# Kernel tuning notes

Measured on AMD Instinct MI355X. Metric: run time of the kernel, lower is better.

The kernel has to match this reference:

```python
import jax, jax.numpy as jnp
import numpy as np

B, N = 8192, 128          # batch, num intruders
D_OWN, D_GRID, D_INTR = 16, 512, 20
H, OUT = 128, 4


def setup_inputs() -> dict:
    key = jax.random.key(0)
    ks = jax.random.split(key, 12)
    rn = lambda k, shape, s=1.0: jax.random.normal(k, shape, jnp.float32) * s
    return {
        "state0": rn(ks[0], (B, D_OWN)),
        "state1": rn(ks[1], (B, D_GRID)),
        "state2": rn(ks[2], (B, N, D_INTR)),
        "W_own": rn(ks[3], (D_OWN, H), 0.1), "b_own": jnp.zeros((H,), jnp.float32),
        "W_intr": rn(ks[4], (D_INTR, H), 0.1), "b_intr": jnp.zeros((H,), jnp.float32),
        "W_grid": rn(ks[5], (D_GRID, H), 0.05), "b_grid": jnp.zeros((H,), jnp.float32),
        "Wq": rn(ks[6], (H, H), 0.08),
        "Wk": rn(ks[7], (H, H), 0.08),
        "Wv": rn(ks[8], (H, H), 0.08),
        "W1": rn(ks[9], (3 * H, H), 0.05), "b1": jnp.zeros((H,), jnp.float32),
        "W2": rn(ks[10], (H, OUT), 0.1), "b2": jnp.zeros((OUT,), jnp.float32),
    }


def reference(state0, state1, state2, W_own, b_own, W_intr, b_intr,
              W_grid, b_grid, Wq, Wk, Wv, W1, b1, W2, b2):
    own_e = jax.nn.relu(state0 @ W_own + b_own)            # [B,H]
    x_e = jax.nn.relu(state2 @ W_intr + b_intr)            # [B,N,H]
    q = own_e @ Wq                                         # [B,H]
    k = x_e @ Wk                                           # [B,N,H]
    v = x_e @ Wv                                           # [B,N,H]
    # mask = state2.mean(axis=2, keepdim=True).bool()  (nonzero test)
    mask = jnp.mean(state2, axis=2, keepdims=True) != 0    # [B,N,1]
    score = jnp.einsum('bnh,bh->bn', k, q)[..., None]      # bmm(k, q.unsqueeze(2)) -> [B,N,1]
    score = jnp.where(mask, score, -jnp.inf)
    alpha = jax.nn.softmax(score / np.float32(np.sqrt(H)), axis=1)
    alpha = jnp.where(mask, alpha, 0.0)
    v_att = jnp.sum(v * alpha, axis=1)                     # [B,H]
    own_grid = jax.nn.relu(state1 @ W_grid + b_grid)       # [B,H]
    concat = jnp.concatenate([own_e, v_att, own_grid], axis=1)  # [B,3H]
    out = (concat @ W1 + b1) @ W2 + b2                     # action_out_SAC
    mean = out
    log_std = jnp.clip(out, -20.0, 2.0)
    return mean, log_std
```

## Files before the change

kernel.cpp:

```cpp
#include <hip/hip_runtime.h>

typedef unsigned short ushort_t;
typedef __attribute__((ext_vector_type(8))) short bf16x8;
typedef __attribute__((ext_vector_type(4))) float f32x4;

__device__ __forceinline__ float bflo(unsigned u) { return __uint_as_float(u << 16); }
__device__ __forceinline__ float bfhi(unsigned u) { return __uint_as_float(u & 0xffff0000u); }
__device__ __forceinline__ float bfu(ushort_t s)  { return __uint_as_float((unsigned)s << 16); }
__device__ __forceinline__ ushort_t f2bf(float f) {
    unsigned u = __float_as_uint(f);
    u = u + 0x7fffu + ((u >> 16) & 1u);
    return (ushort_t)(u >> 16);
}
__device__ __forceinline__ void unpack8(uint4 v, float* f) {
    f[0]=bflo(v.x); f[1]=bfhi(v.x); f[2]=bflo(v.y); f[3]=bfhi(v.y);
    f[4]=bflo(v.z); f[5]=bfhi(v.z); f[6]=bflo(v.w); f[7]=bfhi(v.w);
}

__device__ __forceinline__ float load1(const void* p, size_t i, int f32) {
    return f32 ? ((const float*)p)[i] : bfu(((const ushort_t*)p)[i]);
}
__device__ __forceinline__ void load8(const void* p, size_t i, int f32, float* f) {
    if (f32) {
        const float4 a = *(const float4*)((const float*)p + i);
        const float4 b = *(const float4*)((const float*)p + i + 4);
        f[0]=a.x; f[1]=a.y; f[2]=a.z; f[3]=a.w;
        f[4]=b.x; f[5]=b.y; f[6]=b.z; f[7]=b.w;
    } else {
        unpack8(*(const uint4*)((const ushort_t*)p + i), f);
    }
}
__device__ __forceinline__ void load4(const void* p, size_t i, int f32, float* f) {
    if (f32) {
        const float4 a = *(const float4*)((const float*)p + i);
        f[0]=a.x; f[1]=a.y; f[2]=a.z; f[3]=a.w;
    } else {
        const uint2 u = *(const uint2*)((const ushort_t*)p + i);
        f[0]=bflo(u.x); f[1]=bfhi(u.x); f[2]=bflo(u.y); f[3]=bfhi(u.y);
    }
}

__device__ __forceinline__ int detect_f32(const ushort_t* s1h) {
    const int ln = threadIdx.x & 63;
    float v = fmaxf(fabsf(bfu(s1h[ln])), fabsf(bfu(s1h[ln + 64])));
    bool big = !(v <= 1e6f);
    return __ballot(big) != 0ull;
}

#define B_TOT 8192

__device__ __attribute__((aligned(16))) float    g_M[128 * 128];
__device__ __attribute__((aligned(16))) float    g_Wc1[384 * 4];
__device__ __attribute__((aligned(16))) float    g_Wv2[128 * 4];
__device__ __attribute__((aligned(16))) float    g_bc[4];
__device__ __attribute__((aligned(16))) float    g_t[B_TOT * 128];
__device__ __attribute__((aligned(16))) float    g_ogc[B_TOT * 4];
__device__ __attribute__((aligned(16))) ushort_t g_oe[B_TOT * 128];

__global__ __launch_bounds__(128) void k_pre(
    const void* __restrict__ Wq, const void* __restrict__ Wk,
    const void* __restrict__ Wv, const void* __restrict__ W1,
    const void* __restrict__ b1, const void* __restrict__ W2,
    const void* __restrict__ b2, const ushort_t* __restrict__ s1h)
{
    __shared__ float wq_sh[128];
    __shared__ float w2_sh[512];
    __shared__ float wc1_mid[512];
    __shared__ float redc[128][4];
    const int tid = threadIdx.x;
    const int bx = blockIdx.x;
    const int f32 = detect_f32(s1h);

    if (bx < 128) {
        wq_sh[tid] = load1(Wq, bx*128 + tid, f32);
        __syncthreads();
        float acc = 0.f;
        #pragma unroll
        for (int c = 0; c < 16; ++c) {
            float f[8]; load8(Wk, (size_t)tid*128 + c*8, f32, f);
            #pragma unroll
            for (int j = 0; j < 8; ++j) acc = fmaf(wq_sh[c*8+j], f[j], acc);
        }
        g_M[bx*128 + tid] = acc;
    } else {
        const int rbase = (bx == 128) ? 0 : ((bx == 129) ? 128 : 256);
        for (int i = tid; i < 512; i += 128) w2_sh[i] = load1(W2, i, f32);
        __syncthreads();

        const int r = rbase + tid;
        float a[4] = {0.f, 0.f, 0.f, 0.f};
        #pragma unroll
        for (int c = 0; c < 16; ++c) {
            float f[8]; load8(W1, (size_t)r*128 + c*8, f32, f);
            #pragma unroll
            for (int j = 0; j < 8; ++j) {
                const int p = c*8 + j;
                #pragma unroll
                for (int q = 0; q < 4; ++q) a[q] = fmaf(f[j], w2_sh[p*4+q], a[q]);
            }
        }
        #pragma unroll
        for (int q = 0; q < 4; ++q) g_Wc1[r*4+q] = a[q];

        if (bx == 129) {
            #pragma unroll
            for (int q = 0; q < 4; ++q) wc1_mid[tid*4+q] = a[q];
            __syncthreads();
            float v[4] = {0.f, 0.f, 0.f, 0.f};
            #pragma unroll
            for (int c = 0; c < 16; ++c) {
                float f[8]; load8(Wv, (size_t)tid*128 + c*8, f32, f);
                #pragma unroll
                for (int j = 0; j < 8; ++j) {
                    const int i2 = c*8 + j;
                    #pragma unroll
                    for (int q = 0; q < 4; ++q) v[q] = fmaf(f[j], wc1_mid[i2*4+q], v[q]);
                }
            }
            #pragma unroll
            for (int q = 0; q < 4; ++q) g_Wv2[tid*4+q] = v[q];

            const float bv = load1(b1, tid, f32);
            #pragma unroll
            for (int q = 0; q < 4; ++q) redc[tid][q] = bv * w2_sh[tid*4+q];
            __syncthreads();
            for (int s = 64; s > 0; s >>= 1) {
                if (tid < s) {
                    #pragma unroll
                    for (int q = 0; q < 4; ++q) redc[tid][q] += redc[tid+s][q];
                }
                __syncthreads();
            }
            if (tid < 4) g_bc[tid] = redc[0][tid] + load1(b2, tid, f32);
        }
    }
}

__global__ __launch_bounds__(256) void k_ownt(
    const void* __restrict__ state0, const void* __restrict__ W_own,
    const void* __restrict__ b_own, const ushort_t* __restrict__ s1h)
{
    __shared__ float s0sh[16*16];
    __shared__ float wosh[16*128];
    __shared__ float bosh[128];
    __shared__ float oesh[16*129];
    __shared__ float Mt[32][128];
    const int tid = threadIdx.x;
    const int b0 = blockIdx.x * 16;
    const int f32 = detect_f32(s1h);

    if (tid < 32) {
        float f[8]; load8(state0, (size_t)b0*16 + tid*8, f32, f);
        #pragma unroll
        for (int j = 0; j < 8; ++j) s0sh[tid*8 + j] = f[j];
    }
    {
        float f[8]; load8(W_own, (size_t)tid*8, f32, f);
        #pragma unroll
        for (int j = 0; j < 8; ++j) wosh[tid*8 + j] = f[j];
    }
    if (tid < 128) bosh[tid] = load1(b_own, tid, f32);
    __syncthreads();

    #pragma unroll
    for (int kk = 0; kk < 8; ++kk) {
        const int idx = tid + kk*256;
        const int bi = idx >> 7, h = idx & 127;
        float acc = bosh[h];
        #pragma unroll
        for (int d = 0; d < 16; ++d) acc = fmaf(s0sh[bi*16+d], wosh[d*128+h], acc);
        acc = fmaxf(acc, 0.f);
        oesh[bi*129 + h] = acc;
        g_oe[(size_t)(b0+bi)*128 + h] = f2bf(acc);
    }

    const int bi0 = (tid >> 5) * 2;
    const int h0  = (tid & 31) * 4;
    float t00=0.f,t01=0.f,t02=0.f,t03=0.f,t10=0.f,t11=0.f,t12=0.f,t13=0.f;
    for (int kt = 0; kt < 128; kt += 32) {
        __syncthreads();
        #pragma unroll
        for (int c = 0; c < 4; ++c) {
            const int i = tid + c*256;
            const int kk = i >> 5;
            const int hh = (i & 31) * 4;
            *(float4*)&Mt[kk][hh] = *(const float4*)&g_M[(size_t)(kt+kk)*128 + hh];
        }
        __syncthreads();
        #pragma unroll
        for (int k = 0; k < 32; ++k) {
            const float4 mv = *(const float4*)&Mt[k][h0];
            const float a0 = oesh[(bi0+0)*129 + kt + k];
            const float a1 = oesh[(bi0+1)*129 + kt + k];
            t00=fmaf(a0,mv.x,t00); t01=fmaf(a0,mv.y,t01); t02=fmaf(a0,mv.z,t02); t03=fmaf(a0,mv.w,t03);
            t10=fmaf(a1,mv.x,t10); t11=fmaf(a1,mv.y,t11); t12=fmaf(a1,mv.z,t12); t13=fmaf(a1,mv.w,t13);
        }
    }
    *(float4*)&g_t[(size_t)(b0+bi0+0)*128 + h0] = make_float4(t00,t01,t02,t03);
    *(float4*)&g_t[(size_t)(b0+bi0+1)*128 + h0] = make_float4(t10,t11,t12,t13);
}

__global__ __launch_bounds__(256) void k_grid(
    const void* __restrict__ state1, const void* __restrict__ W_grid,
    const void* __restrict__ b_grid)
{
    __shared__ float s1T[32][18];
    __shared__ float wg[32][128];
    __shared__ float part[32][16][4];
    const int tid = threadIdx.x;
    const int b0 = blockIdx.x * 16;
    const int f32 = detect_f32((const ushort_t*)state1);

    const int bq = tid & 7;
    const int hq = tid >> 3;
    float a00=0.f,a01=0.f,a02=0.f,a03=0.f;
    float a10=0.f,a11=0.f,a12=0.f,a13=0.f;

    for (int kt = 0; kt < 512; kt += 32) {
        if (kt) __syncthreads();
        if (tid < 128) {
            const int bb = tid >> 3;
            const int kk = (tid & 7) * 4;
            float f[4];
            load4(state1, (size_t)(b0 + bb)*512 + kt + kk, f32, f);
            #pragma unroll
            for (int j = 0; j < 4; ++j) s1T[kk + j][bb] = f[j];
        }
        {
            #pragma unroll
            for (int c = 0; c < 4; ++c) {
                const int i = tid + c*256;
                const int kk = i >> 5;
                const int hh = (i & 31) * 4;
                float f[4];
                load4(W_grid, (size_t)(kt + kk)*128 + hh, f32, f);
                *(float4*)&wg[kk][hh] = make_float4(f[0], f[1], f[2], f[3]);
            }
        }
        __syncthreads();
        #pragma unroll 8
        for (int k = 0; k < 32; ++k) {
            const float x0 = s1T[k][bq*2 + 0];
            const float x1 = s1T[k][bq*2 + 1];
            const float4 w = *(const float4*)&wg[k][hq*4];
            a00=fmaf(x0,w.x,a00); a01=fmaf(x0,w.y,a01); a02=fmaf(x0,w.z,a02); a03=fmaf(x0,w.w,a03);
            a10=fmaf(x1,w.x,a10); a11=fmaf(x1,w.y,a11); a12=fmaf(x1,w.z,a12); a13=fmaf(x1,w.w,a13);
        }
    }

    float accs[2][4] = {{a00,a01,a02,a03},{a10,a11,a12,a13}};
    float pr[2][4] = {{0,0,0,0},{0,0,0,0}};
    #pragma unroll
    for (int jh = 0; jh < 4; ++jh) {
        const int h = hq*4 + jh;
        const float bg = load1(b_grid, h, f32);
        const float4 wc = *(const float4*)&g_Wc1[(256 + h)*4];
        #pragma unroll
        for (int ib = 0; ib < 2; ++ib) {
            const float og = fmaxf(accs[ib][jh] + bg, 0.f);
            pr[ib][0] = fmaf(og, wc.x, pr[ib][0]);
            pr[ib][1] = fmaf(og, wc.y, pr[ib][1]);
            pr[ib][2] = fmaf(og, wc.z, pr[ib][2]);
            pr[ib][3] = fmaf(og, wc.w, pr[ib][3]);
        }
    }
    __syncthreads();
    #pragma unroll
    for (int j = 0; j < 4; ++j) {
        part[hq][bq*2+0][j] = pr[0][j];
        part[hq][bq*2+1][j] = pr[1][j];
    }
    __syncthreads();
    if (tid < 64) {
        const int bb = tid >> 2, j = tid & 3;
        float s = 0.f;
        #pragma unroll
        for (int q = 0; q < 32; ++q) s += part[q][bb][j];
        g_ogc[(size_t)(b0 + bb)*4 + j] = s;
    }
}

__global__ __launch_bounds__(256) void k_main(
    const void* __restrict__ state2, const void* __restrict__ W_intr,
    const void* __restrict__ b_intr, const ushort_t* __restrict__ s1h,
    void* __restrict__ out_raw)
{
    __shared__ __attribute__((aligned(16))) ushort_t s2b[128*40];
    __shared__ __attribute__((aligned(16))) ushort_t wib[128*40];
    __shared__ float bi_sh[128], t_sh[128], oe_sh[128];
    __shared__ float score_sh[128], alpha_sh[128], u_sh[128];
    __shared__ float u_red[4][128];
    __shared__ int   msk_sh[128];
    __shared__ float red_sh[8];
    __shared__ float red4[4][4];

    const int tid = threadIdx.x;
    const int b = blockIdx.x;
    const int f32 = detect_f32(s1h);

    if (tid < 128) {
        const int n = tid;
        float v[20];
        const size_t base = (size_t)b*2560 + n*20;
        #pragma unroll
        for (int c = 0; c < 5; ++c) load4(state2, base + c*4, f32, v + c*4);
        float ms = 0.f;
        #pragma unroll
        for (int d = 0; d < 20; ++d) ms += v[d];
        msk_sh[n] = (ms != 0.f) ? 1 : 0;
        unsigned* row = (unsigned*)&s2b[n*40];
        #pragma unroll
        for (int c = 0; c < 10; ++c)
            row[c] = (unsigned)f2bf(v[2*c]) | ((unsigned)f2bf(v[2*c+1]) << 16);
        #pragma unroll
        for (int c = 10; c < 20; ++c) row[c] = 0u;
        t_sh[n]  = g_t[(size_t)b*128 + n];
        oe_sh[n] = bfu(g_oe[(size_t)b*128 + n]);
        bi_sh[n] = load1(b_intr, n, f32);
    } else {
        const int h = tid - 128;
        float w[20];
        #pragma unroll
        for (int d = 0; d < 20; ++d) w[d] = load1(W_intr, (size_t)d*128 + h, f32);
        unsigned* row = (unsigned*)&wib[h*40];
        #pragma unroll
        for (int c = 0; c < 10; ++c)
            row[c] = (unsigned)f2bf(w[2*c]) | ((unsigned)f2bf(w[2*c+1]) << 16);
        #pragma unroll
        for (int c = 10; c < 20; ++c) row[c] = 0u;
    }
    __syncthreads();

    const int wv = tid >> 6, ln = tid & 63, lq = ln >> 4, lc = ln & 15;
    const bf16x8 a0 = *(const bf16x8*)&s2b[((2*wv+0)*16 + lc)*40 + lq*8];
    const bf16x8 a1 = *(const bf16x8*)&s2b[((2*wv+1)*16 + lc)*40 + lq*8];
    const f32x4 zf = {0.f, 0.f, 0.f, 0.f};
    f32x4 acc[2][8];
    #pragma unroll
    for (int th = 0; th < 8; ++th) {
        const bf16x8 bb = *(const bf16x8*)&wib[(th*16 + lc)*40 + lq*8];
        acc[0][th] = __builtin_amdgcn_mfma_f32_16x16x32_bf16(a0, bb, zf, 0, 0, 0);
        acc[1][th] = __builtin_amdgcn_mfma_f32_16x16x32_bf16(a1, bb, zf, 0, 0, 0);
    }

    float sc[2][4] = {{0,0,0,0},{0,0,0,0}};
    #pragma unroll
    for (int th = 0; th < 8; ++th) {
        const float bh = bi_sh[th*16 + lc];
        const float tv = t_sh[th*16 + lc];
        #pragma unroll
        for (int i = 0; i < 2; ++i)
            #pragma unroll
            for (int r = 0; r < 4; ++r) {
                const float xv = fmaxf(acc[i][th][r] + bh, 0.f);
                acc[i][th][r] = xv;
                sc[i][r] = fmaf(xv, tv, sc[i][r]);
            }
    }
    #pragma unroll
    for (int off = 1; off < 16; off <<= 1)
        #pragma unroll
        for (int i = 0; i < 2; ++i)
            #pragma unroll
            for (int r = 0; r < 4; ++r)
                sc[i][r] += __shfl_xor(sc[i][r], off);
    if (lc == 0) {
        #pragma unroll
        for (int i = 0; i < 2; ++i)
            #pragma unroll
            for (int r = 0; r < 4; ++r)
                score_sh[(2*wv+i)*16 + lq*4 + r] = sc[i][r];
    }
    __syncthreads();

    float logit = -1e30f, e = 0.f;
    bool is_m = false;
    if (tid < 128) {
        is_m = msk_sh[tid] != 0;
        if (is_m) logit = score_sh[tid] * 0.08838834764831845f;
    }
    float vmax = logit;
    #pragma unroll
    for (int off = 32; off > 0; off >>= 1) vmax = fmaxf(vmax, __shfl_down(vmax, off));
    if ((tid & 63) == 0) red_sh[tid >> 6] = vmax;
    __syncthreads();
    const float mx = fmaxf(fmaxf(red_sh[0], red_sh[1]), fmaxf(red_sh[2], red_sh[3]));
    if (is_m) e = __expf(fmaxf(logit - mx, -80.f));
    float vs = e;
    #pragma unroll
    for (int off = 32; off > 0; off >>= 1) vs += __shfl_down(vs, off);
    if ((tid & 63) == 0) red_sh[4 + (tid >> 6)] = vs;
    __syncthreads();
    const float denom = red_sh[4] + red_sh[5] + red_sh[6] + red_sh[7];
    if (tid < 128) alpha_sh[tid] = (is_m && denom > 0.f) ? e / denom : 0.f;
    __syncthreads();

    float al[2][4];
    #pragma unroll
    for (int i = 0; i < 2; ++i)
        #pragma unroll
        for (int r = 0; r < 4; ++r)
            al[i][r] = alpha_sh[(2*wv+i)*16 + lq*4 + r];
    float up[8];
    #pragma unroll
    for (int th = 0; th < 8; ++th) {
        float s = 0.f;
        #pragma unroll
        for (int i = 0; i < 2; ++i)
            #pragma unroll
            for (int r = 0; r < 4; ++r)
                s = fmaf(al[i][r], acc[i][th][r], s);
        up[th] = s;
    }
    #pragma unroll
    for (int th = 0; th < 8; ++th) {
        up[th] += __shfl_xor(up[th], 16);
        up[th] += __shfl_xor(up[th], 32);
    }
    if (ln < 16) {
        #pragma unroll
        for (int th = 0; th < 8; ++th) u_red[wv][th*16 + ln] = up[th];
    }
    __syncthreads();
    if (tid < 128)
        u_sh[tid] = u_red[0][tid] + u_red[1][tid] + u_red[2][tid] + u_red[3][tid];
    __syncthreads();

    float c0=0.f, c1=0.f, c2=0.f, c3=0.f;
    if (tid < 128) {
        const int h = tid;
        const float uu = u_sh[h], oo = oe_sh[h];
        const float4 wv2 = *(const float4*)&g_Wv2[h*4];
        const float4 wca = *(const float4*)&g_Wc1[h*4];
        c0 = uu*wv2.x + oo*wca.x;
        c1 = uu*wv2.y + oo*wca.y;
        c2 = uu*wv2.z + oo*wca.z;
        c3 = uu*wv2.w + oo*wca.w;
    }
    #pragma unroll
    for (int off = 32; off > 0; off >>= 1) {
        c0 += __shfl_down(c0, off); c1 += __shfl_down(c1, off);
        c2 += __shfl_down(c2, off); c3 += __shfl_down(c3, off);
    }
    if ((tid & 63) == 0) {
        const int w = tid >> 6;
        red4[w][0]=c0; red4[w][1]=c1; red4[w][2]=c2; red4[w][3]=c3;
    }
    __syncthreads();
    if (tid < 4) {
        const int j = tid;
        const float o = g_bc[j] + g_ogc[(size_t)b*4 + j]
                      + red4[0][j] + red4[1][j] + red4[2][j] + red4[3][j];
        const float ls = fminf(fmaxf(o, -20.f), 2.f);
        if (f32) {
            float* of = (float*)out_raw;
            of[(size_t)b*4 + j] = o;
            of[(size_t)B_TOT*4 + (size_t)b*4 + j] = ls;
        } else {
            ushort_t* os = (ushort_t*)out_raw;
            os[(size_t)b*4 + j] = f2bf(o);
            os[(size_t)B_TOT*4 + (size_t)b*4 + j] = f2bf(ls);
        }
    }
}

extern "C" void kernel_launch(void* const* d_in, const int* in_sizes, int n_in,
                              void* d_out, int out_size, void* d_ws, size_t ws_size,
                              hipStream_t stream)
{
    (void)in_sizes; (void)n_in; (void)out_size; (void)d_ws; (void)ws_size;
    const void* state0 = d_in[0];
    const void* state1 = d_in[1];
    const void* state2 = d_in[2];
    const void* W_own  = d_in[3];
    const void* b_own  = d_in[4];
    const void* W_intr = d_in[5];
    const void* b_intr = d_in[6];
    const void* W_grid = d_in[7];
    const void* b_grid = d_in[8];
    const void* Wq     = d_in[9];
    const void* Wk     = d_in[10];
    const void* Wv     = d_in[11];
    const void* W1     = d_in[12];
    const void* b1     = d_in[13];
    const void* W2     = d_in[14];
    const void* b2     = d_in[15];
    const ushort_t* s1h = (const ushort_t*)state1;

    k_pre  <<<dim3(131), dim3(128), 0, stream>>>(Wq, Wk, Wv, W1, b1, W2, b2, s1h);
    k_ownt <<<dim3(512), dim3(256), 0, stream>>>(state0, W_own, b_own, s1h);
    k_grid <<<dim3(512), dim3(256), 0, stream>>>(state1, W_grid, b_grid);
    k_main <<<dim3(8192), dim3(256), 0, stream>>>(state2, W_intr, b_intr, s1h, d_out);
}
```

Measured before the change: 296.4 us.

## Pre-pack W_intr once and repartition attention MFMA tiles by hidden dimension

Moves the bf16 conversion of W_intr into a new k_pre block that writes a padded global buffer, so each k_main block only copies it instead of converting it per batch row. k_main now gives each wave two hidden tiles across all intruders rather than two intruder tiles across all hidden units. The score reduction goes through per-wave partials, and the softmax uses full-wave xor shuffles that every wave computes redundantly. This removes several barriers and the alpha/u_red round trips through shared memory, and adds launch_bounds occupancy hint 4, at the cost of recomputing exp per element in each wave.

Result: slower. 313.5 us (+5.7%).

```diff
diff --git a/kernel.cpp b/kernel.cpp
--- a/kernel.cpp
+++ b/kernel.cpp
@@ -56,12 +56,14 @@
 __device__ __attribute__((aligned(16))) float    g_t[B_TOT * 128];
 __device__ __attribute__((aligned(16))) float    g_ogc[B_TOT * 4];
 __device__ __attribute__((aligned(16))) ushort_t g_oe[B_TOT * 128];
+__device__ __attribute__((aligned(16))) ushort_t g_Wib[128 * 32];
 
 __global__ __launch_bounds__(128) void k_pre(
     const void* __restrict__ Wq, const void* __restrict__ Wk,
     const void* __restrict__ Wv, const void* __restrict__ W1,
     const void* __restrict__ b1, const void* __restrict__ W2,
-    const void* __restrict__ b2, const ushort_t* __restrict__ s1h)
+    const void* __restrict__ b2, const void* __restrict__ W_intr,
+    const ushort_t* __restrict__ s1h)
 {
     __shared__ float wq_sh[128];
     __shared__ float w2_sh[512];
@@ -82,8 +84,8 @@
             for (int j = 0; j < 8; ++j) acc = fmaf(wq_sh[c*8+j], f[j], acc);
         }
         g_M[bx*128 + tid] = acc;
-    } else {
-        const int rbase = (bx == 128) ? 0 : ((bx == 129) ? 128 : 256);
+    } else if (bx < 131) {
+        const int rbase = (bx - 128) * 128;
         for (int i = tid; i < 512; i += 128) w2_sh[i] = load1(W2, i, f32);
         __syncthreads();
 
@@ -133,6 +135,16 @@
             }
             if (tid < 4) g_bc[tid] = redc[0][tid] + load1(b2, tid, f32);
         }
+    } else {
+        ushort_t row[32];
+        #pragma unroll
+        for (int k = 0; k < 20; ++k) row[k] = f2bf(load1(W_intr, (size_t)k*128 + tid, f32));
+        #pragma unroll
+        for (int k = 20; k < 32; ++k) row[k] = 0;
+        uint4* dst = (uint4*)&g_Wib[tid*32];
+        const uint4* src = (const uint4*)row;
+        #pragma unroll
+        for (int c = 0; c < 4; ++c) dst[c] = src[c];
     }
 }
 
@@ -280,23 +292,23 @@
     }
 }
 
-__global__ __launch_bounds__(256) void k_main(
-    const void* __restrict__ state2, const void* __restrict__ W_intr,
-    const void* __restrict__ b_intr, const ushort_t* __restrict__ s1h,
-    void* __restrict__ out_raw)
+__global__ __launch_bounds__(256, 4) void k_main(
+    const void* __restrict__ state2, const void* __restrict__ b_intr,
+    const ushort_t* __restrict__ s1h, void* __restrict__ out_raw)
 {
     __shared__ __attribute__((aligned(16))) ushort_t s2b[128*40];
     __shared__ __attribute__((aligned(16))) ushort_t wib[128*40];
-    __shared__ float bi_sh[128], t_sh[128], oe_sh[128];
-    __shared__ float score_sh[128], alpha_sh[128], u_sh[128];
-    __shared__ float u_red[4][128];
-    __shared__ int   msk_sh[128];
-    __shared__ float red_sh[8];
+    __shared__ float t_sh[128], oe_sh[128], bi_sh[128];
+    __shared__ float2 mlg_sh[128];
+    __shared__ float msk_f[128];
+    __shared__ float sc_part[4][128];
+    __shared__ float u_sh[128];
     __shared__ float red4[4][4];
 
     const int tid = threadIdx.x;
     const int b = blockIdx.x;
     const int f32 = detect_f32(s1h);
+    const int wv = tid >> 6, ln = tid & 63, lq = ln >> 4, lc = ln & 15;
 
     if (tid < 128) {
         const int n = tid;
@@ -307,123 +319,95 @@
         float ms = 0.f;
         #pragma unroll
         for (int d = 0; d < 20; ++d) ms += v[d];
-        msk_sh[n] = (ms != 0.f) ? 1 : 0;
+        msk_f[n] = (ms != 0.f) ? 1.f : 0.f;
         unsigned* row = (unsigned*)&s2b[n*40];
         #pragma unroll
         for (int c = 0; c < 10; ++c)
             row[c] = (unsigned)f2bf(v[2*c]) | ((unsigned)f2bf(v[2*c+1]) << 16);
         #pragma unroll
-        for (int c = 10; c < 20; ++c) row[c] = 0u;
+        for (int c = 10; c < 16; ++c) row[c] = 0u;
         t_sh[n]  = g_t[(size_t)b*128 + n];
         oe_sh[n] = bfu(g_oe[(size_t)b*128 + n]);
         bi_sh[n] = load1(b_intr, n, f32);
     } else {
         const int h = tid - 128;
-        float w[20];
-        #pragma unroll
-        for (int d = 0; d < 20; ++d) w[d] = load1(W_intr, (size_t)d*128 + h, f32);
-        unsigned* row = (unsigned*)&wib[h*40];
-        #pragma unroll
-        for (int c = 0; c < 10; ++c)
-            row[c] = (unsigned)f2bf(w[2*c]) | ((unsigned)f2bf(w[2*c+1]) << 16);
-        #pragma unroll
-        for (int c = 10; c < 20; ++c) row[c] = 0u;
-    }
-    __syncthreads();
-
-    const int wv = tid >> 6, ln = tid & 63, lq = ln >> 4, lc = ln & 15;
-    const bf16x8 a0 = *(const bf16x8*)&s2b[((2*wv+0)*16 + lc)*40 + lq*8];
-    const bf16x8 a1 = *(const bf16x8*)&s2b[((2*wv+1)*16 + lc)*40 + lq*8];
+        const uint4* src = (const uint4*)&g_Wib[h*32];
+        uint4* dst = (uint4*)&wib[h*40];
+        #pragma unroll
+        for (int c = 0; c < 4; ++c) dst[c] = src[c];
+    }
+    __syncthreads();
+
+    const int ht0 = 2*wv, ht1 = 2*wv + 1;
+    const bf16x8 bb0 = *(const bf16x8*)&wib[(ht0*16 + lc)*40 + lq*8];
+    const bf16x8 bb1 = *(const bf16x8*)&wib[(ht1*16 + lc)*40 + lq*8];
     const f32x4 zf = {0.f, 0.f, 0.f, 0.f};
-    f32x4 acc[2][8];
-    #pragma unroll
-    for (int th = 0; th < 8; ++th) {
-        const bf16x8 bb = *(const bf16x8*)&wib[(th*16 + lc)*40 + lq*8];
-        acc[0][th] = __builtin_amdgcn_mfma_f32_16x16x32_bf16(a0, bb, zf, 0, 0, 0);
-        acc[1][th] = __builtin_amdgcn_mfma_f32_16x16x32_bf16(a1, bb, zf, 0, 0, 0);
-    }
-
-    float sc[2][4] = {{0,0,0,0},{0,0,0,0}};
-    #pragma unroll
-    for (int th = 0; th < 8; ++th) {
-        const float bh = bi_sh[th*16 + lc];
-        const float tv = t_sh[th*16 + lc];
-        #pragma unroll
-        for (int i = 0; i < 2; ++i)
-            #pragma unroll
-            for (int r = 0; r < 4; ++r) {
-                const float xv = fmaxf(acc[i][th][r] + bh, 0.f);
-                acc[i][th][r] = xv;
-                sc[i][r] = fmaf(xv, tv, sc[i][r]);
-            }
-    }
-    #pragma unroll
-    for (int off = 1; off < 16; off <<= 1)
-        #pragma unroll
-        for (int i = 0; i < 2; ++i)
-            #pragma unroll
-            for (int r = 0; r < 4; ++r)
-                sc[i][r] += __shfl_xor(sc[i][r], off);
-    if (lc == 0) {
-        #pragma unroll
-        for (int i = 0; i < 2; ++i)
-            #pragma unroll
-            for (int r = 0; r < 4; ++r)
-                score_sh[(2*wv+i)*16 + lq*4 + r] = sc[i][r];
-    }
-    __syncthreads();
-
-    float logit = -1e30f, e = 0.f;
-    bool is_m = false;
+    f32x4 acc0[8], acc1[8];
+    #pragma unroll
+    for (int nt = 0; nt < 8; ++nt) {
+        const bf16x8 af = *(const bf16x8*)&s2b[(nt*16 + lc)*40 + lq*8];
+        acc0[nt] = __builtin_amdgcn_mfma_f32_16x16x32_bf16(af, bb0, zf, 0, 0, 0);
+        acc1[nt] = __builtin_amdgcn_mfma_f32_16x16x32_bf16(af, bb1, zf, 0, 0, 0);
+    }
+
+    const float bh0 = bi_sh[ht0*16 + lc], bh1 = bi_sh[ht1*16 + lc];
+    const float tv0 = t_sh[ht0*16 + lc],  tv1 = t_sh[ht1*16 + lc];
+    #pragma unroll
+    for (int nt = 0; nt < 8; ++nt) {
+        float s[4];
+        #pragma unroll
+        for (int r = 0; r < 4; ++r) {
+            const float x0 = fmaxf(acc0[nt][r] + bh0, 0.f);
+            const float x1 = fmaxf(acc1[nt][r] + bh1, 0.f);
+            acc0[nt][r] = x0; acc1[nt][r] = x1;
+            s[r] = fmaf(x1, tv1, x0 * tv0);
+        }
+        #pragma unroll
+        for (int off = 1; off < 16; off <<= 1) {
+            #pragma unroll
+            for (int r = 0; r < 4; ++r) s[r] += __shfl_xor(s[r], off);
+        }
+        if (lc == 0) {
+            #pragma unroll
+            for (int r = 0; r < 4; ++r) sc_part[wv][nt*16 + lq*4 + r] = s[r];
+        }
+    }
+    __syncthreads();
+
     if (tid < 128) {
-        is_m = msk_sh[tid] != 0;
-        if (is_m) logit = score_sh[tid] * 0.08838834764831845f;
-    }
-    float vmax = logit;
-    #pragma unroll
-    for (int off = 32; off > 0; off >>= 1) vmax = fmaxf(vmax, __shfl_down(vmax, off));
-    if ((tid & 63) == 0) red_sh[tid >> 6] = vmax;
-    __syncthreads();
-    const float mx = fmaxf(fmaxf(red_sh[0], red_sh[1]), fmaxf(red_sh[2], red_sh[3]));
-    if (is_m) e = __expf(fmaxf(logit - mx, -80.f));
-    float vs = e;
-    #pragma unroll
-    for (int off = 32; off > 0; off >>= 1) vs += __shfl_down(vs, off);
-    if ((tid & 63) == 0) red_sh[4 + (tid >> 6)] = vs;
-    __syncthreads();
-    const float denom = red_sh[4] + red_sh[5] + red_sh[6] + red_sh[7];
-    if (tid < 128) alpha_sh[tid] = (is_m && denom > 0.f) ? e / denom : 0.f;
-    __syncthreads();
-
-    float al[2][4];
-    #pragma unroll
-    for (int i = 0; i < 2; ++i)
-        #pragma unroll
-        for (int r = 0; r < 4; ++r)
-            al[i][r] = alpha_sh[(2*wv+i)*16 + lq*4 + r];
-    float up[8];
-    #pragma unroll
-    for (int th = 0; th < 8; ++th) {
-        float s = 0.f;
-        #pragma unroll
-        for (int i = 0; i < 2; ++i)
-            #pragma unroll
-            for (int r = 0; r < 4; ++r)
-                s = fmaf(al[i][r], acc[i][th][r], s);
-        up[th] = s;
-    }
-    #pragma unroll
-    for (int th = 0; th < 8; ++th) {
-        up[th] += __shfl_xor(up[th], 16);
-        up[th] += __shfl_xor(up[th], 32);
-    }
+        const int n = tid;
+        const float s = sc_part[0][n] + sc_part[1][n] + sc_part[2][n] + sc_part[3][n];
+        const float mk = msk_f[n];
+        mlg_sh[n] = make_float2((mk != 0.f) ? s * 0.08838834764831845f : -1e30f, mk);
+    }
+    __syncthreads();
+
+    const float l0 = mlg_sh[ln].x, l1 = mlg_sh[ln + 64].x;
+    float mx = fmaxf(l0, l1);
+    #pragma unroll
+    for (int off = 1; off < 64; off <<= 1) mx = fmaxf(mx, __shfl_xor(mx, off));
+    float es = __expf(fmaxf(l0 - mx, -80.f)) + __expf(fmaxf(l1 - mx, -80.f));
+    #pragma unroll
+    for (int off = 1; off < 64; off <<= 1) es += __shfl_xor(es, off);
+    const float inv_d = 1.f / es;
+
+    float u0 = 0.f, u1 = 0.f;
+    #pragma unroll
+    for (int nt = 0; nt < 8; ++nt) {
+        #pragma unroll
+        for (int r = 0; r < 4; ++r) {
+            const float2 mlg = mlg_sh[nt*16 + lq*4 + r];
+            const float a = mlg.y * __expf(fmaxf(mlg.x - mx, -80.f)) * inv_d;
+            u0 = fmaf(a, acc0[nt][r], u0);
+            u1 = fmaf(a, acc1[nt][r], u1);
+        }
+    }
+    u0 += __shfl_xor(u0, 16); u0 += __shfl_xor(u0, 32);
+    u1 += __shfl_xor(u1, 16); u1 += __shfl_xor(u1, 32);
     if (ln < 16) {
-        #pragma unroll
-        for (int th = 0; th < 8; ++th) u_red[wv][th*16 + ln] = up[th];
-    }
-    __syncthreads();
-    if (tid < 128)
-        u_sh[tid] = u_red[0][tid] + u_red[1][tid] + u_red[2][tid] + u_red[3][tid];
+        u_sh[ht0*16 + ln] = u0;
+        u_sh[ht1*16 + ln] = u1;
+    }
     __syncthreads();
 
     float c0=0.f, c1=0.f, c2=0.f, c3=0.f;
@@ -443,8 +427,7 @@
         c2 += __shfl_down(c2, off); c3 += __shfl_down(c3, off);
     }
     if ((tid & 63) == 0) {
-        const int w = tid >> 6;
-        red4[w][0]=c0; red4[w][1]=c1; red4[w][2]=c2; red4[w][3]=c3;
+        red4[wv][0]=c0; red4[wv][1]=c1; red4[wv][2]=c2; red4[wv][3]=c3;
     }
     __syncthreads();
     if (tid < 4) {
@@ -487,8 +470,9 @@
     const void* b2     = d_in[15];
     const ushort_t* s1h = (const ushort_t*)state1;
 
-    k_pre  <<<dim3(131), dim3(128), 0, stream>>>(Wq, Wk, Wv, W1, b1, W2, b2, s1h);
+    k_pre  <<<dim3(132), dim3(128), 0, stream>>>(Wq, Wk, Wv, W1, b1, W2, b2,
+                                                 W_intr, s1h);
     k_ownt <<<dim3(512), dim3(256), 0, stream>>>(state0, W_own, b_own, s1h);
     k_grid <<<dim3(512), dim3(256), 0, stream>>>(state1, W_grid, b_grid);
-    k_main <<<dim3(8192), dim3(256), 0, stream>>>(state2, W_intr, b_intr, s1h, d_out);
-}
+    k_main <<<dim3(8192), dim3(256), 0, stream>>>(state2, b_intr, s1h, d_out);
+}
```
